# Performance work log

Hardware: AMD Instinct MI355X
Metric: run time of the kernel (lower is better)

Reference implementation:

```python
import jax, jax.numpy as jnp
import numpy as np

D = 768        # d_model
NH = 12        # num_heads
HD = D // NH   # head_dim = 64
MH = 3072      # mlp_hidden = 4*d_model
EPS = 1e-5
SCALE = HD ** -0.5


def _ln(x, w, b):
    m = jnp.mean(x, axis=-1, keepdims=True)
    v = jnp.mean(jnp.square(x - m), axis=-1, keepdims=True)
    return (x - m) * jax.lax.rsqrt(v + EPS) * w + b


def _rotate_half(x):
    x1, x2 = jnp.split(x, 2, axis=-1)
    return jnp.concatenate([-x2, x1], axis=-1)


def _rope_cos_sin(n, dim):
    inv = 1.0 / (10000.0 ** (jnp.arange(0, dim, 2, dtype=jnp.float32) / dim))
    ang = jnp.arange(n, dtype=jnp.float32)[:, None] * inv[None, :]
    ang = jnp.concatenate([ang, ang], axis=-1)  # (n, dim)
    return jnp.cos(ang), jnp.sin(ang)


def _mlp(x, w1, b1, w2, b2):
    return jax.nn.gelu(x @ w1 + b1, approximate=False) @ w2 + b2


def _attn(q, k, v):
    # q,k,v: (B, S, NH, HD)
    a = jnp.einsum('bqhd,bkhd->bhqk', q, k) * SCALE
    a = jax.nn.softmax(a, axis=-1)
    return jnp.einsum('bhqk,bkhd->bqhd', a, v)


def _spatial_attn(x, qkv_w, proj_w, proj_b):
    # x: (B, T, H, W, C); attention over H*W per frame with 2D RoPE
    B, T, H, W, C = x.shape
    BT, S = B * T, H * W
    qkv = x.reshape(BT, S, C) @ qkv_w
    q, k, v = jnp.split(qkv, 3, axis=-1)
    q = q.reshape(BT, S, NH, HD)
    k = k.reshape(BT, S, NH, HD)
    v = v.reshape(BT, S, NH, HD)
    half = HD // 2
    cos_h, sin_h = _rope_cos_sin(H, half)
    cos_w, sin_w = _rope_cos_sin(W, half)

    def rope2d(t):
        t = t.reshape(BT, H, W, NH, HD)
        t1, t2 = t[..., :half], t[..., half:]
        ch, sh = cos_h[None, :, None, None, :], sin_h[None, :, None, None, :]
        cw, sw = cos_w[None, None, :, None, :], sin_w[None, None, :, None, :]
        t1 = t1 * ch + _rotate_half(t1) * sh  # rotate by row position
        t2 = t2 * cw + _rotate_half(t2) * sw  # rotate by col position
        return jnp.concatenate([t1, t2], axis=-1).reshape(BT, S, NH, HD)

    out = _attn(rope2d(q), rope2d(k), v).reshape(BT, S, C) @ proj_w + proj_b
    return out.reshape(B, T, H, W, C)


def _temporal_attn(vp, vf, ap, af, qkv_w, proj_w, proj_b):
    # vp/vf: (B, T, S, C); ap/af: (B, T, C); joint attention over concatenated time axis
    B, T_p, S, C = vp.shape
    T_f = vf.shape[1]
    BS = B * S
    vps = vp.transpose(0, 2, 1, 3).reshape(BS, T_p, C)
    vfs = vf.transpose(0, 2, 1, 3).reshape(BS, T_f, C)
    aps = jnp.broadcast_to(ap[:, None], (B, S, T_p, C)).reshape(BS, T_p, C)
    afs = jnp.broadcast_to(af[:, None], (B, S, T_f, C)).reshape(BS, T_f, C)
    tok = jnp.concatenate([vps, vfs, aps, afs], axis=1)
    TT = tok.shape[1]
    qkv = tok @ qkv_w
    q, k, v = jnp.split(qkv, 3, axis=-1)
    q = q.reshape(BS, TT, NH, HD)
    k = k.reshape(BS, TT, NH, HD)
    v = v.reshape(BS, TT, NH, HD)
    cos, sin = _rope_cos_sin(TT, HD)
    rope1d = lambda t: t * cos[None, :, None, :] + _rotate_half(t) * sin[None, :, None, :]
    out = _attn(rope1d(q), rope1d(k), v).reshape(BS, TT, C) @ proj_w + proj_b
    vp_o = out[:, :T_p].reshape(B, S, T_p, C).transpose(0, 2, 1, 3)
    vf_o = out[:, T_p:T_p + T_f].reshape(B, S, T_f, C).transpose(0, 2, 1, 3)
    ap_o = out[:, T_p + T_f:T_p + T_f + T_p].reshape(B, S, T_p, C).mean(axis=1)
    af_o = out[:, T_p + T_f + T_p:].reshape(B, S, T_f, C).mean(axis=1)
    return vp_o, vf_o, ap_o, af_o


def _forward(v_p, v_f, a_p, a_f,
             sa_qkv_w, sa_proj_w, sa_proj_b,
             smlp_w1, smlp_b1, smlp_w2, smlp_b2,
             ta_qkv_w, ta_proj_w, ta_proj_b,
             ln1_w, ln1_b, ln2_w, ln2_b, ln3_w, ln3_b, ln4_w, ln4_b,
             fvp_w1, fvp_b1, fvp_w2, fvp_b2,
             fvf_w1, fvf_b1, fvf_w2, fvf_b2,
             fap_w1, fap_b1, fap_w2, fap_b2,
             faf_w1, faf_b1, faf_w2, faf_b2):
    # 1) shared spatial attention (video streams) + 2) shared video MLP, pre-norm residual
    def video_stage(x):
        x = x + _spatial_attn(_ln(x, ln1_w, ln1_b), sa_qkv_w, sa_proj_w, sa_proj_b)
        x = x + _mlp(_ln(x, ln2_w, ln2_b), smlp_w1, smlp_b1, smlp_w2, smlp_b2)
        return x
    v_p = video_stage(v_p)
    v_f = video_stage(v_f)
    B, T_p, H, W, C = v_p.shape
    T_f = v_f.shape[1]
    S = H * W
    vp_s = v_p.reshape(B, T_p, S, C)
    vf_s = v_f.reshape(B, T_f, S, C)
    # 3) joint temporal attention across all streams with 1D RoPE
    dvp, dvf, dap, daf = _temporal_attn(
        _ln(vp_s, ln3_w, ln3_b), _ln(vf_s, ln3_w, ln3_b),
        _ln(a_p, ln3_w, ln3_b), _ln(a_f, ln3_w, ln3_b),
        ta_qkv_w, ta_proj_w, ta_proj_b)
    vp_s = vp_s + dvp
    vf_s = vf_s + dvf
    a_p = a_p + dap
    a_f = a_f + daf
    # 4) distinct final MLP per stream
    vp_s = vp_s + _mlp(_ln(vp_s, ln4_w, ln4_b), fvp_w1, fvp_b1, fvp_w2, fvp_b2)
    vf_s = vf_s + _mlp(_ln(vf_s, ln4_w, ln4_b), fvf_w1, fvf_b1, fvf_w2, fvf_b2)
    a_p = a_p + _mlp(_ln(a_p, ln4_w, ln4_b), fap_w1, fap_b1, fap_w2, fap_b2)
    a_f = a_f + _mlp(_ln(a_f, ln4_w, ln4_b), faf_w1, faf_b1, faf_w2, faf_b2)
    return (vp_s.reshape(B, T_p, H, W, C), vf_s.reshape(B, T_f, H, W, C), a_p, a_f)


def setup_inputs() -> dict:
    B, T, H, W = 4, 8, 16, 16
    key = jax.random.key(0)
    kit = iter(jax.random.split(key, 48))
    def nrm(shape, s=0.02):
        return jax.random.normal(next(kit), shape, jnp.float32) * s
    inp = {
        'v_p': jax.random.normal(next(kit), (B, T, H, W, D), jnp.float32),
        'v_f': jax.random.normal(next(kit), (B, T, H, W, D), jnp.float32),
        'a_p': jax.random.normal(next(kit), (B, T, D), jnp.float32),
        'a_f': jax.random.normal(next(kit), (B, T, D), jnp.float32),
        'sa_qkv_w': nrm((D, 3 * D)),
        'sa_proj_w': nrm((D, D)),
        'sa_proj_b': jnp.zeros((D,), jnp.float32),
        'smlp_w1': nrm((D, MH)), 'smlp_b1': jnp.zeros((MH,), jnp.float32),
        'smlp_w2': nrm((MH, D)), 'smlp_b2': jnp.zeros((D,), jnp.float32),
        'ta_qkv_w': nrm((D, 3 * D)),
        'ta_proj_w': nrm((D, D)),
        'ta_proj_b': jnp.zeros((D,), jnp.float32),
    }
    for nm in ('ln1', 'ln2', 'ln3', 'ln4'):
        inp[nm + '_w'] = jnp.ones((D,), jnp.float32)
        inp[nm + '_b'] = jnp.zeros((D,), jnp.float32)
    for nm in ('fvp', 'fvf', 'fap', 'faf'):
        inp[nm + '_w1'] = nrm((D, MH))
        inp[nm + '_b1'] = jnp.zeros((MH,), jnp.float32)
        inp[nm + '_w2'] = nrm((MH, D))
        inp[nm + '_b2'] = jnp.zeros((D,), jnp.float32)
    return inp


def reference(v_p, v_f, a_p, a_f,
              sa_qkv_w, sa_proj_w, sa_proj_b,
              smlp_w1, smlp_b1, smlp_w2, smlp_b2,
              ta_qkv_w, ta_proj_w, ta_proj_b,
              ln1_w, ln1_b, ln2_w, ln2_b, ln3_w, ln3_b, ln4_w, ln4_b,
              fvp_w1, fvp_b1, fvp_w2, fvp_b2,
              fvf_w1, fvf_b1, fvf_w2, fvf_b2,
              fap_w1, fap_b1, fap_w2, fap_b2,
              faf_w1, faf_b1, faf_w2, faf_b2):
    return _forward(v_p, v_f, a_p, a_f,
                    sa_qkv_w, sa_proj_w, sa_proj_b,
                    smlp_w1, smlp_b1, smlp_w2, smlp_b2,
                    ta_qkv_w, ta_proj_w, ta_proj_b,
                    ln1_w, ln1_b, ln2_w, ln2_b, ln3_w, ln3_b, ln4_w, ln4_b,
                    fvp_w1, fvp_b1, fvp_w2, fvp_b2,
                    fvf_w1, fvf_b1, fvf_w2, fvf_b2,
                    fap_w1, fap_b1, fap_w2, fap_b2,
                    faf_w1, faf_b1, faf_w2, faf_b2)
```

## Files before the change

kernel.cpp:

```cpp
#include <hip/hip_runtime.h>
#include <hip/hip_bf16.h>

#define D 768
#define NH 12
#define HD 64
#define MH 3072
#define LN_EPS 1e-5f
#define ATT_SCALE 0.125f

typedef unsigned short u16;
typedef unsigned int u32;
typedef short short8 __attribute__((ext_vector_type(8)));
typedef float f32x4 __attribute__((ext_vector_type(4)));

__device__ __forceinline__ float b2f(u16 u){
  union { u32 i; float f; } x; x.i = ((u32)u) << 16; return x.f;
}
__device__ __forceinline__ u16 f2b(float f){
  u32 x = __float_as_uint(f);
  x += 0x7fffu + ((x >> 16) & 1u);
  return (u16)(x >> 16);
}
__device__ __forceinline__ u32 packb(float a, float b){
  return (u32)f2b(a) | ((u32)f2b(b) << 16);
}
__device__ __forceinline__ bool is_f32(const u32* __restrict__ probe){
  return probe[0] == 0x3F800000u;
}

__device__ __forceinline__ void gload_lds16(const u16* g, u16* l){
  auto const* gp = reinterpret_cast<u32 const __attribute__((address_space(1)))*>(
      reinterpret_cast<uintptr_t>(g));
  auto* lp = reinterpret_cast<u32 __attribute__((address_space(3)))*>(
      reinterpret_cast<uintptr_t>(l));
  __builtin_amdgcn_global_load_lds(gp, lp, 16, 0, 0);
}

__device__ __forceinline__ void up8(uint4 u, float* f){
  f[0] = b2f((u16)(u.x & 0xffff)); f[1] = b2f((u16)(u.x >> 16));
  f[2] = b2f((u16)(u.y & 0xffff)); f[3] = b2f((u16)(u.y >> 16));
  f[4] = b2f((u16)(u.z & 0xffff)); f[5] = b2f((u16)(u.z >> 16));
  f[6] = b2f((u16)(u.w & 0xffff)); f[7] = b2f((u16)(u.w >> 16));
}

__global__ void k_in2f(const void* __restrict__ in, float* __restrict__ out, int n4,
                       const u32* __restrict__ probe){
  int i = blockIdx.x * 256 + threadIdx.x;
  if (i >= n4) return;
  if (is_f32(probe)){
    ((float4*)out)[i] = ((const float4*)in)[i];
  } else {
    uint2 u = ((const uint2*)in)[i];
    float4 f;
    f.x = b2f((u16)(u.x & 0xffff)); f.y = b2f((u16)(u.x >> 16));
    f.z = b2f((u16)(u.y & 0xffff)); f.w = b2f((u16)(u.y >> 16));
    ((float4*)out)[i] = f;
  }
}

__global__ void k_out(const float* __restrict__ in, void* __restrict__ out,
                      size_t elem_off, int n4, const u32* __restrict__ probe){
  int i = blockIdx.x * 256 + threadIdx.x;
  if (i >= n4) return;
  float4 f = ((const float4*)in)[i];
  if (is_f32(probe)){
    ((float4*)((float*)out + elem_off))[i] = f;
  } else {
    uint2 u;
    u.x = packb(f.x, f.y);
    u.y = packb(f.z, f.w);
    ((uint2*)((u16*)out + elem_off))[i] = u;
  }
}

__global__ __launch_bounds__(256) void k_transp(const void* __restrict__ W,
    u16* __restrict__ WT, int K, int N, const u32* __restrict__ probe)
{
  __shared__ u16 t[32][33];
  bool wf = is_f32(probe);
  int k0 = blockIdx.x * 32, n0 = blockIdx.y * 32;
  int tx = threadIdx.x & 31, ty = threadIdx.x >> 5;
  #pragma unroll
  for (int i = 0; i < 4; i++){
    int k = k0 + ty + i*8;
    float v = wf ? ((const float*)W)[(size_t)k*N + n0 + tx]
                 : b2f(((const u16*)W)[(size_t)k*N + n0 + tx]);
    t[ty + i*8][tx] = f2b(v);
  }
  __syncthreads();
  #pragma unroll
  for (int i = 0; i < 4; i++){
    int n = n0 + ty + i*8;
    WT[(size_t)n*K + k0 + tx] = t[tx][ty + i*8];
  }
}

__global__ __launch_bounds__(256) void k_ln(const float* __restrict__ X,
    const void* __restrict__ w, const void* __restrict__ b,
    u16* __restrict__ Y, int nrows, const u32* __restrict__ probe)
{
  bool wf = is_f32(probe);
  int wv = threadIdx.x >> 6, lane = threadIdx.x & 63;
  int row = blockIdx.x * 4 + wv;
  if (row >= nrows) return;
  const float* x = X + (size_t)row * D;
  float v[12];
  float s = 0.f;
  #pragma unroll
  for (int i = 0; i < 12; i++){ v[i] = x[lane + i*64]; s += v[i]; }
  #pragma unroll
  for (int m = 32; m; m >>= 1) s += __shfl_xor(s, m);
  float mean = s * (1.f/768.f);
  float q = 0.f;
  #pragma unroll
  for (int i = 0; i < 12; i++){ float d0 = v[i] - mean; q += d0*d0; }
  #pragma unroll
  for (int m = 32; m; m >>= 1) q += __shfl_xor(q, m);
  float rstd = rsqrtf(q * (1.f/768.f) + LN_EPS);
  u16* y = Y + (size_t)row * D;
  #pragma unroll
  for (int i = 0; i < 12; i++){
    int c = lane + i*64;
    float wc = wf ? ((const float*)w)[c] : b2f(((const u16*)w)[c]);
    float bc = wf ? ((const float*)b)[c] : b2f(((const u16*)b)[c]);
    y[c] = f2b((v[i] - mean) * rstd * wc + bc);
  }
}

#define BM 128
#define BK 64

template<int EPI, int GUARD, int BNN>
__global__ __launch_bounds__(256, 2) void k_gemm(
    const u16* __restrict__ A, const u16* __restrict__ WT,
    const void* __restrict__ bias, void* __restrict__ Cout,
    const float* __restrict__ resid, const u32* __restrict__ probe,
    int M, int N, int K)
{
  constexpr int AT = (BNN == 128) ? 4 : 2;
  __shared__ __align__(16) u16 lA[2][BM][BK];
  __shared__ __align__(16) u16 lB[2][BNN][BK];
  bool wf = is_f32(probe);
  int tid = threadIdx.x;
  int m0 = blockIdx.y * BM, n0 = blockIdx.x * BNN;
  int wv = tid >> 6, lane = tid & 63, quad = lane >> 4, r = lane & 15;
  int wm = (BNN == 128) ? (wv >> 1) * 64 : wv * 32;
  int wn = (BNN == 128) ? (wv & 1) * 64 : 0;

  f32x4 acc[AT][4] = {};

  int lrow = lane >> 3;
  int scol = ((lane & 7) ^ lrow) * 8;
  int nt = K / BK;

  auto stage = [&](int t, int bi){
    int k0 = t * BK;
    if (GUARD){
      int a_r = tid >> 3;
      int a_sl = tid & 7;
      #pragma unroll
      for (int p = 0; p < 4; p++){
        int row = p*32 + a_r;
        uint4 val = make_uint4(0u,0u,0u,0u);
        if (m0 + row < M)
          val = *(const uint4*)(A + (size_t)(m0+row)*K + k0 + a_sl*8);
        *(uint4*)&lA[bi][row][(a_sl ^ (row & 7)) * 8] = val;
      }
    } else {
      #pragma unroll
      for (int p = 0; p < 4; p++){
        int c = wv*4 + p;
        gload_lds16(A + (size_t)(m0 + c*8 + lrow)*K + k0 + scol, &lA[bi][c*8][0]);
      }
    }
    #pragma unroll
    for (int p = 0; p < BNN/32; p++){
      int c = wv*(BNN/32) + p;
      gload_lds16(WT + (size_t)(n0 + c*8 + lrow)*K + k0 + scol, &lB[bi][c*8][0]);
    }
  };

  stage(0, 0);
  __syncthreads();

  for (int t = 0; t < nt; ++t){
    int cur = t & 1;
    if (t + 1 < nt) stage(t + 1, cur ^ 1);
    #pragma unroll
    for (int kk = 0; kk < 2; kk++){
      short8 af[AT], bf[4];
      #pragma unroll
      for (int i = 0; i < AT; i++)
        af[i] = *(const short8*)&lA[cur][wm + i*16 + r][((kk*4 + quad) ^ (r & 7)) * 8];
      #pragma unroll
      for (int j = 0; j < 4; j++)
        bf[j] = *(const short8*)&lB[cur][wn + j*16 + r][((kk*4 + quad) ^ (r & 7)) * 8];
      #pragma unroll
      for (int i = 0; i < AT; i++)
        #pragma unroll
        for (int j = 0; j < 4; j++)
          acc[i][j] = __builtin_amdgcn_mfma_f32_16x16x32_bf16(af[i], bf[j], acc[i][j], 0, 0, 0);
    }
    __syncthreads();
  }

  #pragma unroll
  for (int i = 0; i < AT; i++){
    #pragma unroll
    for (int reg = 0; reg < 4; reg++){
      int row = m0 + wm + i*16 + quad*4 + reg;
      if (row >= M) continue;
      #pragma unroll
      for (int j = 0; j < 4; j++){
        int col = n0 + wn + j*16 + r;
        float v = acc[i][j][reg];
        size_t idx = (size_t)row * N + col;
        if (EPI == 0){
          ((u16*)Cout)[idx] = f2b(v);
        } else if (EPI == 1){
          v += wf ? ((const float*)bias)[col] : b2f(((const u16*)bias)[col]);
          v = 0.5f * v * (1.f + erff(v * 0.70710678f));
          ((u16*)Cout)[idx] = f2b(v);
        } else {
          v += (wf ? ((const float*)bias)[col] : b2f(((const u16*)bias)[col])) + resid[idx];
          ((float*)Cout)[idx] = v;
        }
      }
    }
  }
}

__global__ __launch_bounds__(512, 2) void k_spat_attn(
    const u16* __restrict__ QKV, u16* __restrict__ OUT)
{
  __shared__ __align__(16) u16 lK[256*64];
  __shared__ __align__(16) u16 lVT[64*256];
  __shared__ __align__(16) u16 lQP[256*64];
  int bt = blockIdx.x / NH, h = blockIdx.x % NH;
  int tid = threadIdx.x;

  {
    int token = tid >> 1, half = tid & 1;
    int dbase = half * 32;
    float pos = half ? (float)(token & 15) : (float)(token >> 4);
    const u16* src = QKV + (size_t)(bt*256 + token) * 2304 + h*64 + dbase;
    float q[32], k[32];
    #pragma unroll
    for (int i = 0; i < 4; i++){
      up8(((const uint4*)src)[i],         &q[i*8]);
      up8(((const uint4*)(src + 768))[i], &k[i*8]);
    }
    #pragma unroll
    for (int j = 0; j < 16; j++){
      float inv = exp2f(-(float)j * 0.8304820237721841f);
      float sn, cs; __sincosf(pos * inv, &sn, &cs);
      { float a = q[j], b = q[j+16]; q[j] = a*cs - b*sn; q[j+16] = b*cs + a*sn; }
      { float a = k[j], b = k[j+16]; k[j] = a*cs - b*sn; k[j+16] = b*cs + a*sn; }
    }
    #pragma unroll
    for (int g = 0; g < 4; g++){
      int slot = (half*4 + g) ^ (token & 7);
      u32 wq[4], wk[4];
      #pragma unroll
      for (int p2 = 0; p2 < 4; p2++){
        wq[p2] = packb(q[g*8+p2*2] * ATT_SCALE, q[g*8+p2*2+1] * ATT_SCALE);
        wk[p2] = packb(k[g*8+p2*2], k[g*8+p2*2+1]);
      }
      *(uint4*)&lQP[token*64 + slot*8] = *(uint4*)wq;
      *(uint4*)&lK [token*64 + slot*8] = *(uint4*)wk;
    }
    uint4 vv[4];
    #pragma unroll
    for (int i = 0; i < 4; i++) vv[i] = ((const uint4*)(src + 1536))[i];
    #pragma unroll
    for (int i = 0; i < 32; i++){
      int d = dbase + i;
      u32 w = ((const u32*)vv)[i >> 1];
      lVT[d*256 + (((token>>3) ^ (d&7))*8) + (token&7)] =
          (i & 1) ? (u16)(w >> 16) : (u16)(w & 0xffff);
    }
  }
  __syncthreads();

  int wv = tid >> 6, lane = tid & 63, quad = lane >> 4, r = lane & 15;

  short8 qa[2][2];
  #pragma unroll
  for (int qt = 0; qt < 2; qt++)
    #pragma unroll
    for (int dc = 0; dc < 2; dc++){
      int q = wv*32 + qt*16 + r;
      int slot = (dc*4 + quad) ^ (q & 7);
      qa[qt][dc] = *(const short8*)&lQP[q*64 + slot*8];
    }
  __syncthreads();

  u16* Pw = &lQP[wv * 1024];
  const short8 ones = {(short)0x3F80,(short)0x3F80,(short)0x3F80,(short)0x3F80,
                       (short)0x3F80,(short)0x3F80,(short)0x3F80,(short)0x3F80};
  f32x4 acc[2][4] = {};
  f32x4 lacc[2] = {};
  float mrow[2][4];
  #pragma unroll
  for (int qt = 0; qt < 2; qt++)
    #pragma unroll
    for (int rg = 0; rg < 4; rg++) mrow[qt][rg] = -1e30f;

  for (int c = 0; c < 8; c++){
    f32x4 s[2][2] = {};
    #pragma unroll
    for (int dc = 0; dc < 2; dc++){
      short8 bk[2];
      #pragma unroll
      for (int kt = 0; kt < 2; kt++){
        int kk = c*32 + kt*16 + r;
        int slot = (dc*4 + quad) ^ (kk & 7);
        bk[kt] = *(const short8*)&lK[kk*64 + slot*8];
      }
      #pragma unroll
      for (int qt = 0; qt < 2; qt++)
        #pragma unroll
        for (int kt = 0; kt < 2; kt++)
          s[qt][kt] = __builtin_amdgcn_mfma_f32_16x16x32_bf16(qa[qt][dc], bk[kt], s[qt][kt], 0, 0, 0);
    }
    #pragma unroll
    for (int qt = 0; qt < 2; qt++){
      float corr[4];
      #pragma unroll
      for (int rg = 0; rg < 4; rg++){
        float mx = fmaxf(s[qt][0][rg], s[qt][1][rg]);
        #pragma unroll
        for (int msk = 1; msk <= 8; msk <<= 1) mx = fmaxf(mx, __shfl_xor(mx, msk));
        float mn = fmaxf(mrow[qt][rg], mx);
        corr[rg] = __expf(mrow[qt][rg] - mn);
        mrow[qt][rg] = mn;
      }
      #pragma unroll
      for (int rg = 0; rg < 4; rg++) lacc[qt][rg] *= corr[rg];
      #pragma unroll
      for (int dt = 0; dt < 4; dt++)
        #pragma unroll
        for (int rg = 0; rg < 4; rg++) acc[qt][dt][rg] *= corr[rg];
      #pragma unroll
      for (int kt = 0; kt < 2; kt++)
        #pragma unroll
        for (int rg = 0; rg < 4; rg++){
          float p = __expf(s[qt][kt][rg] - mrow[qt][rg]);
          int qq = qt*16 + quad*4 + rg;
          int kk = kt*16 + r;
          Pw[qq*32 + (((kk>>3) ^ ((qq>>1)&3))*8) + (kk&7)] = f2b(p);
        }
    }
    short8 pa[2];
    #pragma unroll
    for (int qt = 0; qt < 2; qt++){
      int qq = qt*16 + r;
      int slot = quad ^ ((qq>>1)&3);
      pa[qt] = *(const short8*)&Pw[qq*32 + slot*8];
      lacc[qt] = __builtin_amdgcn_mfma_f32_16x16x32_bf16(pa[qt], ones, lacc[qt], 0, 0, 0);
    }
    #pragma unroll
    for (int dt = 0; dt < 4; dt++){
      int d = dt*16 + r;
      int slot = (c*4 + quad) ^ (d & 7);
      short8 bv = *(const short8*)&lVT[d*256 + slot*8];
      #pragma unroll
      for (int qt = 0; qt < 2; qt++)
        acc[qt][dt] = __builtin_amdgcn_mfma_f32_16x16x32_bf16(pa[qt], bv, acc[qt][dt], 0, 0, 0);
    }
  }

  #pragma unroll
  for (int qt = 0; qt < 2; qt++)
    #pragma unroll
    for (int rg = 0; rg < 4; rg++){
      float invl = 1.f / lacc[qt][rg];
      int row = bt*256 + wv*32 + qt*16 + quad*4 + rg;
      u16* dst = OUT + (size_t)row * 768 + h*64;
      #pragma unroll
      for (int dt = 0; dt < 4; dt++)
        dst[dt*16 + r] = f2b(acc[qt][dt][rg] * invl);
    }
}

__global__ __launch_bounds__(256, 2) void k_temp_attn(
    const u16* __restrict__ QKVv, const u16* __restrict__ QKVa,
    u16* __restrict__ OUTv, u16* __restrict__ SCR)
{
  __shared__ __align__(16) u16 lQP[4][32*64];
  __shared__ __align__(16) u16 lK [4][32*64];
  __shared__ __align__(16) u16 lVT[4][64*32];
  int bs = blockIdx.x; int b = bs >> 8, s = bs & 255;
  int tid = threadIdx.x;
  int wv = tid >> 6, lane = tid & 63, quad = lane >> 4, r = lane & 15;
  int t = lane >> 1, half = lane & 1;
  int dA = half*16, dB = half*16 + 32;

  const u16* rowp;
  if (t < 8)       rowp = QKVv + (size_t)((b*8 + t)*256 + s) * 2304;
  else if (t < 16) rowp = QKVv + (size_t)(8192 + (b*8 + t-8)*256 + s) * 2304;
  else if (t < 24) rowp = QKVa + (size_t)(b*8 + t-16) * 2304;
  else             rowp = QKVa + (size_t)(32 + b*8 + t-24) * 2304;

  float rsn[16], rcs[16];
  #pragma unroll
  for (int dd = 0; dd < 16; dd++){
    int j = dA + dd;
    float inv = exp2f(-(float)j * 0.4152410118860920f);
    __sincosf((float)t * inv, &rsn[dd], &rcs[dd]);
  }

  u16* Qw = lQP[wv]; u16* Kw = lK[wv]; u16* VTw = lVT[wv];

  #pragma unroll 1
  for (int hi = 0; hi < 3; hi++){
    int h = wv*3 + hi;
    const u16* src = rowp + h*64;

    {
      float qa_[32], ka_[32];
      up8(((const uint4*)(src + dA))[0],       &qa_[0]);
      up8(((const uint4*)(src + dA))[1],       &qa_[8]);
      up8(((const uint4*)(src + dB))[0],       &qa_[16]);
      up8(((const uint4*)(src + dB))[1],       &qa_[24]);
      up8(((const uint4*)(src + 768 + dA))[0], &ka_[0]);
      up8(((const uint4*)(src + 768 + dA))[1], &ka_[8]);
      up8(((const uint4*)(src + 768 + dB))[0], &ka_[16]);
      up8(((const uint4*)(src + 768 + dB))[1], &ka_[24]);
      #pragma unroll
      for (int dd = 0; dd < 16; dd++){
        float a = qa_[dd], p = qa_[16+dd];
        qa_[dd]    = a*rcs[dd] - p*rsn[dd];
        qa_[16+dd] = p*rcs[dd] + a*rsn[dd];
        float c = ka_[dd], d2 = ka_[16+dd];
        ka_[dd]    = c*rcs[dd] - d2*rsn[dd];
        ka_[16+dd] = d2*rcs[dd] + c*rsn[dd];
      }
      u32 wq[16], wk[16];
      #pragma unroll
      for (int p = 0; p < 16; p++){
        wq[p] = packb(qa_[2*p]*ATT_SCALE, qa_[2*p+1]*ATT_SCALE);
        wk[p] = packb(ka_[2*p],           ka_[2*p+1]);
      }
      #pragma unroll
      for (int g = 0; g < 4; g++){
        int sl = ((g & 1) + ((g >> 1) << 2) + half*2) ^ (t & 7);
        *(uint4*)&Qw[t*64 + sl*8] = *(uint4*)&wq[g*4];
        *(uint4*)&Kw[t*64 + sl*8] = *(uint4*)&wk[g*4];
      }
    }
    {
      u32 vw[16];
      *(uint4*)&vw[0]  = ((const uint4*)(src + 1536 + dA))[0];
      *(uint4*)&vw[4]  = ((const uint4*)(src + 1536 + dA))[1];
      *(uint4*)&vw[8]  = ((const uint4*)(src + 1536 + dB))[0];
      *(uint4*)&vw[12] = ((const uint4*)(src + 1536 + dB))[1];
      #pragma unroll
      for (int i = 0; i < 32; i++){
        int d = (i < 16) ? (dA + i) : (dB + i - 16);
        u16 val = (i & 1) ? (u16)(vw[i>>1] >> 16) : (u16)(vw[i>>1] & 0xffff);
        VTw[d*32 + (((t>>3) ^ (d&3))*8) + (t&7)] = val;
      }
    }

    short8 qa[2][2];
    #pragma unroll
    for (int qt = 0; qt < 2; qt++)
      #pragma unroll
      for (int dc = 0; dc < 2; dc++){
        int q = qt*16 + r;
        int slot = (dc*4 + quad) ^ (q & 7);
        qa[qt][dc] = *(const short8*)&Qw[q*64 + slot*8];
      }
    f32x4 sv[2][2] = {};
    #pragma unroll
    for (int dc = 0; dc < 2; dc++){
      short8 bk[2];
      #pragma unroll
      for (int kt = 0; kt < 2; kt++){
        int kk = kt*16 + r;
        int slot = (dc*4 + quad) ^ (kk & 7);
        bk[kt] = *(const short8*)&Kw[kk*64 + slot*8];
      }
      #pragma unroll
      for (int qt = 0; qt < 2; qt++)
        #pragma unroll
        for (int kt = 0; kt < 2; kt++)
          sv[qt][kt] = __builtin_amdgcn_mfma_f32_16x16x32_bf16(qa[qt][dc], bk[kt], sv[qt][kt], 0, 0, 0);
    }

    u16* Pw = Qw;
    float linv[2][4];
    #pragma unroll
    for (int qt = 0; qt < 2; qt++){
      #pragma unroll
      for (int rg = 0; rg < 4; rg++){
        float mx = fmaxf(sv[qt][0][rg], sv[qt][1][rg]);
        #pragma unroll
        for (int msk = 1; msk <= 8; msk <<= 1) mx = fmaxf(mx, __shfl_xor(mx, msk));
        int qq = qt*16 + quad*4 + rg;
        float sum = 0.f;
        #pragma unroll
        for (int kt = 0; kt < 2; kt++){
          float p = __expf(sv[qt][kt][rg] - mx);
          u16 pq = f2b(p);
          sum += b2f(pq);
          int kk = kt*16 + r;
          Pw[qq*32 + (((kk>>3) ^ ((qq>>1)&3))*8) + (kk&7)] = pq;
        }
        #pragma unroll
        for (int msk = 1; msk <= 8; msk <<= 1) sum += __shfl_xor(sum, msk);
        linv[qt][rg] = 1.f / sum;
      }
    }

    short8 pa[2];
    #pragma unroll
    for (int qt = 0; qt < 2; qt++){
      int qq = qt*16 + r;
      int slot = quad ^ ((qq>>1)&3);
      pa[qt] = *(const short8*)&Pw[qq*32 + slot*8];
    }
    f32x4 oacc[2][4] = {};
    #pragma unroll
    for (int dt = 0; dt < 4; dt++){
      int d = dt*16 + r;
      int slot = quad ^ (d & 3);
      short8 bv = *(const short8*)&VTw[d*32 + slot*8];
      #pragma unroll
      for (int qt = 0; qt < 2; qt++)
        oacc[qt][dt] = __builtin_amdgcn_mfma_f32_16x16x32_bf16(pa[qt], bv, oacc[qt][dt], 0, 0, 0);
    }

    #pragma unroll
    for (int rg = 0; rg < 4; rg++){
      int token = quad*4 + rg;
      size_t orow = (token < 8) ? (size_t)((b*8 + token)*256 + s)
                                : (size_t)(8192 + (b*8 + token-8)*256 + s);
      u16* dst = OUTv + orow*768 + h*64;
      #pragma unroll
      for (int dt = 0; dt < 4; dt++)
        dst[dt*16 + r] = f2b(oacc[0][dt][rg] * linv[0][rg]);
    }
    #pragma unroll
    for (int rg = 0; rg < 4; rg++){
      int token = quad*4 + rg;
      u16* dst = SCR + ((size_t)bs*16 + token)*768 + h*64;
      #pragma unroll
      for (int dt = 0; dt < 4; dt++)
        dst[dt*16 + r] = f2b(oacc[1][dt][rg] * linv[1][rg]);
    }
  }
}

__global__ void k_audio_reduce(const u16* __restrict__ SCR, u16* __restrict__ OUT){
  int r = blockIdx.x;
  int b, tok;
  if (r < 32){ b = r >> 3; tok = r & 7; }
  else       { int rr = r - 32; b = rr >> 3; tok = 8 + (rr & 7); }
  for (int d = threadIdx.x; d < 768; d += 256){
    float acc = 0.f;
    for (int s2 = 0; s2 < 256; s2++)
      acc += b2f(SCR[((size_t)(b*256 + s2)*16 + tok)*768 + d]);
    OUT[(size_t)r*768 + d] = f2b(acc * (1.f/256.f));
  }
}

extern "C" void kernel_launch(void* const* d_in, const int* in_sizes, int n_in,
                              void* d_out, int out_size, void* d_ws, size_t ws_size,
                              hipStream_t stream)
{
  (void)in_sizes; (void)n_in; (void)out_size; (void)ws_size;
  const void* v_p_i    = d_in[0];
  const void* v_f_i    = d_in[1];
  const void* a_p_i    = d_in[2];
  const void* a_f_i    = d_in[3];
  const void* sa_qkv_w = d_in[4];
  const void* sa_proj_w= d_in[5];
  const void* sa_proj_b= d_in[6];
  const void* smlp_w1  = d_in[7];
  const void* smlp_b1  = d_in[8];
  const void* smlp_w2  = d_in[9];
  const void* smlp_b2  = d_in[10];
  const void* ta_qkv_w = d_in[11];
  const void* ta_proj_w= d_in[12];
  const void* ta_proj_b= d_in[13];
  const void* ln1_w = d_in[14];
  const void* ln1_b = d_in[15];
  const void* ln2_w = d_in[16];
  const void* ln2_b = d_in[17];
  const void* ln3_w = d_in[18];
  const void* ln3_b = d_in[19];
  const void* ln4_w = d_in[20];
  const void* ln4_b = d_in[21];
  const void* fvp_w1= d_in[22];
  const void* fvp_b1= d_in[23];
  const void* fvp_w2= d_in[24];
  const void* fvp_b2= d_in[25];
  const void* fvf_w1= d_in[26];
  const void* fvf_b1= d_in[27];
  const void* fvf_w2= d_in[28];
  const void* fvf_b2= d_in[29];
  const void* fap_w1= d_in[30];
  const void* fap_b1= d_in[31];
  const void* fap_w2= d_in[32];
  const void* fap_b2= d_in[33];
  const void* faf_w1= d_in[34];
  const void* faf_b1= d_in[35];
  const void* faf_w2= d_in[36];
  const void* faf_b2= d_in[37];
  const u32* probe = (const u32*)ln1_w;

  char* ws = (char*)d_ws;
  float* XP  = (float*)(ws + 0);
  float* XF  = (float*)(ws + 25165824);
  float* AP  = (float*)(ws + 50331648);
  float* AF  = (float*)(ws + 50429952);
  u16*  LN   = (u16*)(ws + 50528256);
  u16*  SCR  = LN;
  u16*  QKV  = (u16*)(ws + 75694080);
  u16*  HB   = QKV;
  u16*  HB16 = QKV;
  u16*  ATTN = (u16*)(ws + 151191552);
  u16*  ALN  = (u16*)(ws + 176357376);
  u16*  AQKV = (u16*)(ws + 176455680);
  u16*  AATT = (u16*)(ws + 176750592);
  u16*  AH   = (u16*)(ws + 176848896);
  u16*  WT_SAQKV = (u16*)(ws + 177242112);
  u16*  WT_SAPRJ = (u16*)(ws + 180781056);
  u16*  WT_SMLP1 = (u16*)(ws + 181960704);
  u16*  WT_SMLP2 = (u16*)(ws + 186679296);
  u16*  WTS      = (u16*)(ws + 191397888);

  auto transp = [&](const void* Wm, u16* WT, int K, int N){
    dim3 g(K/32, N/32);
    k_transp<<<g, 256, 0, stream>>>(Wm, WT, K, N, probe);
  };

  auto gemm = [&](int EPI_, const u16* Ap, const u16* WTp, const void* bias,
                  void* Cp, const float* resid, int M, int N, int K){
    bool g = (M % 128) != 0;
    bool n64 = ((size_t)(N/128)) * ((M+127)/128) < 512;
    dim3 grid(N / (n64 ? 64 : 128), (M+127)/128);
    #define LG(E,G,B) k_gemm<E,G,B><<<grid,256,0,stream>>>(Ap,WTp,bias,Cp,resid,probe,M,N,K)
    if (EPI_ == 0){
      if (g){ if (n64) LG(0,1,64); else LG(0,1,128); }
      else  { if (n64) LG(0,0,64); else LG(0,0,128); }
    } else if (EPI_ == 1){
      if (g){ if (n64) LG(1,1,64); else LG(1,1,128); }
      else  { if (n64) LG(1,0,64); else LG(1,0,128); }
    } else {
      if (g){ if (n64) LG(2,1,64); else LG(2,1,128); }
      else  { if (n64) LG(2,0,64); else LG(2,0,128); }
    }
    #undef LG
  };
  auto gemm0 = [&](const u16* A, const u16* WT, u16* C, int M, int N, int K){
    gemm(0, A, WT, (const void*)nullptr, (void*)C, (const float*)nullptr, M, N, K);
  };
  auto gemm1 = [&](const u16* A, const u16* WT, const void* bias, u16* C, int M, int N, int K){
    gemm(1, A, WT, bias, (void*)C, (const float*)nullptr, M, N, K);
  };
  auto gemm2 = [&](const u16* A, const u16* WT, const void* bias, float* C, int M, int N, int K){
    gemm(2, A, WT, bias, (void*)C, (const float*)C, M, N, K);
  };

  transp(sa_qkv_w,  WT_SAQKV, 768, 2304);
  transp(sa_proj_w, WT_SAPRJ, 768, 768);
  transp(smlp_w1,   WT_SMLP1, 768, 3072);
  transp(smlp_w2,   WT_SMLP2, 3072, 768);

  k_in2f<<<6144, 256, 0, stream>>>(v_p_i, XP, 6291456/4, probe);
  k_in2f<<<6144, 256, 0, stream>>>(v_f_i, XF, 6291456/4, probe);
  k_ln<<<4096, 256, 0, stream>>>(XP, ln1_w, ln1_b, LN, 16384, probe);
  gemm0(LN, WT_SAQKV, QKV, 16384, 2304, 768);
  k_spat_attn<<<768, 512, 0, stream>>>(QKV, ATTN);
  gemm2(ATTN, WT_SAPRJ, sa_proj_b, XP, 16384, 768, 768);
  k_ln<<<4096, 256, 0, stream>>>(XP, ln2_w, ln2_b, LN, 16384, probe);
  gemm1(LN, WT_SMLP1, smlp_b1, HB16, 16384, 3072, 768);
  gemm2(HB16, WT_SMLP2, smlp_b2, XP, 16384, 768, 3072);

  k_in2f<<<24, 256, 0, stream>>>(a_p_i, AP, 24576/4, probe);
  k_in2f<<<24, 256, 0, stream>>>(a_f_i, AF, 24576/4, probe);
  k_ln<<<4096, 256, 0, stream>>>(XP, ln3_w, ln3_b, LN, 16384, probe);
  k_ln<<<16, 256, 0, stream>>>(AP, ln3_w, ln3_b, ALN, 64, probe);
  transp(ta_qkv_w, WTS, 768, 2304);
  gemm0(LN, WTS, QKV, 16384, 2304, 768);
  gemm0(ALN, WTS, AQKV, 64, 2304, 768);
  k_temp_attn<<<1024, 256, 0, stream>>>(QKV, AQKV, ATTN, SCR);
  k_audio_reduce<<<64, 256, 0, stream>>>(SCR, AATT);
  transp(ta_proj_w, WTS, 768, 768);
  gemm2(ATTN, WTS, ta_proj_b, XP, 16384, 768, 768);
  gemm2(AATT, WTS, ta_proj_b, AP, 64, 768, 768);

  k_ln<<<4096, 256, 0, stream>>>(XP, ln4_w, ln4_b, LN, 16384, probe);
  k_ln<<<16, 256, 0, stream>>>(AP, ln4_w, ln4_b, ALN, 64, probe);
  transp(fvp_w1, WTS, 768, 3072);
  gemm1(LN, WTS, fvp_b1, HB, 8192, 3072, 768);
  transp(fvp_w2, WTS, 3072, 768);
  gemm2(HB, WTS, fvp_b2, XP, 8192, 768, 3072);
  transp(fvf_w1, WTS, 768, 3072);
  gemm1(LN + (size_t)8192*768, WTS, fvf_b1, HB, 8192, 3072, 768);
  transp(fvf_w2, WTS, 3072, 768);
  gemm2(HB, WTS, fvf_b2, XF, 8192, 768, 3072);
  transp(fap_w1, WTS, 768, 3072);
  gemm1(ALN, WTS, fap_b1, AH, 32, 3072, 768);
  transp(fap_w2, WTS, 3072, 768);
  gemm2(AH, WTS, fap_b2, AP, 32, 768, 3072);
  transp(faf_w1, WTS, 768, 3072);
  gemm1(ALN + (size_t)32*768, WTS, faf_b1, AH, 32, 3072, 768);
  transp(faf_w2, WTS, 3072, 768);
  gemm2(AH, WTS, faf_b2, AF, 32, 768, 3072);

  k_out<<<12288, 256, 0, stream>>>(XP, d_out, 0,        12582912/4, probe);
  k_out<<<48,    256, 0, stream>>>(AP, d_out, 12582912, 49152/4,    probe);
}
```

Before: 1.641 ms.

## Overlap GEMM tile loads with compute via partial vmcnt waits and XCD-aware block remap

Replaces the full __syncthreads after each prefetch with an explicit s_waitcnt vmcnt that waits only for the current tile's direct-to-LDS loads, so the next tile's loads stay in flight during MFMA compute. It also remaps workgroup indices so consecutive tiles land on the same XCD for better L2 reuse, and drops the guarded path to a single LDS buffer, which may raise occupancy there. The hand-counted vmcnt values depend on the exact number of loads per stage, so a miscount could race on LDS.

Measured after the change: 1.527 ms. 7.0% less time.

```diff
diff --git a/kernel.cpp b/kernel.cpp
--- a/kernel.cpp
+++ b/kernel.cpp
@@ -138,11 +138,22 @@
     int M, int N, int K)
 {
   constexpr int AT = (BNN == 128) ? 4 : 2;
-  __shared__ __align__(16) u16 lA[2][BM][BK];
-  __shared__ __align__(16) u16 lB[2][BNN][BK];
+  constexpr int NB = GUARD ? 1 : 2;
+  constexpr int LL = (BNN == 128) ? 8 : 6;
+  __shared__ __align__(16) u16 lA[NB][BM][BK];
+  __shared__ __align__(16) u16 lB[NB][BNN][BK];
   bool wf = is_f32(probe);
   int tid = threadIdx.x;
-  int m0 = blockIdx.y * BM, n0 = blockIdx.x * BNN;
+
+  int gx = gridDim.x;
+  int nwg = gx * gridDim.y;
+  int flat = blockIdx.y * gx + blockIdx.x;
+  if ((nwg & 7) == 0){
+    int cpx = nwg >> 3;
+    flat = (flat & 7) * cpx + (flat >> 3);
+  }
+  int m0 = (flat / gx) * BM, n0 = (flat % gx) * BNN;
+
   int wv = tid >> 6, lane = tid & 63, quad = lane >> 4, r = lane & 15;
   int wm = (BNN == 128) ? (wv >> 1) * 64 : wv * 32;
   int wn = (BNN == 128) ? (wv & 1) * 64 : 0;
@@ -180,28 +191,45 @@
     }
   };
 
-  stage(0, 0);
-  __syncthreads();
-
-  for (int t = 0; t < nt; ++t){
-    int cur = t & 1;
-    if (t + 1 < nt) stage(t + 1, cur ^ 1);
+  auto compute = [&](int bi){
     #pragma unroll
     for (int kk = 0; kk < 2; kk++){
       short8 af[AT], bf[4];
       #pragma unroll
       for (int i = 0; i < AT; i++)
-        af[i] = *(const short8*)&lA[cur][wm + i*16 + r][((kk*4 + quad) ^ (r & 7)) * 8];
+        af[i] = *(const short8*)&lA[bi][wm + i*16 + r][((kk*4 + quad) ^ (r & 7)) * 8];
       #pragma unroll
       for (int j = 0; j < 4; j++)
-        bf[j] = *(const short8*)&lB[cur][wn + j*16 + r][((kk*4 + quad) ^ (r & 7)) * 8];
+        bf[j] = *(const short8*)&lB[bi][wn + j*16 + r][((kk*4 + quad) ^ (r & 7)) * 8];
       #pragma unroll
       for (int i = 0; i < AT; i++)
         #pragma unroll
         for (int j = 0; j < 4; j++)
           acc[i][j] = __builtin_amdgcn_mfma_f32_16x16x32_bf16(af[i], bf[j], acc[i][j], 0, 0, 0);
     }
-    __syncthreads();
+  };
+
+  if (GUARD){
+    for (int t = 0; t < nt; ++t){
+      __syncthreads();
+      stage(t, 0);
+      __syncthreads();
+      compute(0);
+    }
+  } else {
+    stage(0, 0);
+    for (int t = 0; t < nt; ++t){
+      int cur = t & 1;
+      if (t + 1 < nt){
+        stage(t + 1, cur ^ 1);
+        asm volatile("s_waitcnt vmcnt(%0)" :: "i"(LL) : "memory");
+      } else {
+        asm volatile("s_waitcnt vmcnt(0)" ::: "memory");
+      }
+      __builtin_amdgcn_s_barrier();
+      compute(cur);
+      __builtin_amdgcn_s_barrier();
+    }
   }
 
   #pragma unroll
```
